# Optimization experiments

Measured on AMD Instinct MI355X. Metric: run time of the kernel, lower is better.

## Reference

```python
import jax, jax.numpy as jnp
import numpy as np

L = 10


def setup_inputs() -> dict:
    key = jax.random.key(0)
    ks = jax.random.split(key, L + 1)
    N = 1_000_000
    inp = {"points": jax.random.normal(ks[0], (N, 3), dtype=jnp.float32)}
    inp["cob_1"] = jax.random.normal(ks[1], (3, 3), dtype=jnp.float32)
    for l in range(2, L + 1):
        # [2l+1, 3*(2l-1)] change-of-basis matrix for angular order l
        inp[f"cob_{l}"] = jax.random.normal(ks[l], (2 * l + 1, 3 * (2 * l - 1)), dtype=jnp.float32)
    return inp


def _harmonic_forward(points, cobs):
    # points: [..., 3]; cobs: list of L matrices (cob_1 .. cob_L)
    shape = points.shape[:-1]
    f0 = jnp.ones(shape + (1,), dtype=points.dtype)
    # order-1 feature: [..., 3]
    f1 = jnp.einsum('...i,ji->...j', points, cobs[0])
    feats = [f0, f1]
    prev = f1
    for l in range(2, L + 1):
        cob = cobs[l - 1]  # [2l+1, 3*(2l-1)]
        # outer product of previous order feature with order-1 feature, flattened
        f = jnp.einsum('...i,...j->...ij', prev, f1).reshape(shape + (-1,))  # [..., 3*(2l-1)]
        f = jnp.einsum('...i,ji->...j', f, cob)  # [..., 2l+1]
        feats.append(f)
        prev = f
    return jnp.concatenate(feats, axis=-1)  # [..., (L+1)^2]


def reference(points, cob_1, cob_2, cob_3, cob_4, cob_5, cob_6, cob_7, cob_8, cob_9, cob_10):
    cobs = [cob_1, cob_2, cob_3, cob_4, cob_5, cob_6, cob_7, cob_8, cob_9, cob_10]
    return _harmonic_forward(points, cobs)
```

## Files before the change

kernel.cpp:

```cpp
#include <hip/hip_runtime.h>

#define BS 64
#define NFEAT 121
#define CHUNK 16
#define NCHUNK 4


__device__ __forceinline__ float dot3(const float* __restrict__ c, float x, float y, float z) {
    return fmaf(c[2], z, fmaf(c[1], y, c[0] * x));
}

template<int LL>
__device__ __forceinline__ void step_l(const float* __restrict__ cob,
                                       float* f, float f1x, float f1y, float f1z) {
    constexpr int IN = 2 * LL - 1;
    constexpr int OUT = 2 * LL + 1;
    constexpr int PB = (LL - 1) * (LL - 1);
    constexpr int OB = LL * LL;
    #pragma unroll
    for (int j = 0; j < OUT; ++j) {
        const float* __restrict__ crow = cob + j * (3 * IN);
        float acc = 0.f;
        #pragma unroll
        for (int a = 0; a < IN; ++a)
            acc = fmaf(f[PB + a], dot3(crow + 3 * a, f1x, f1y, f1z), acc);
        f[OB + j] = acc;
    }
}

__global__ __launch_bounds__(BS) void harmonic_kernel(
    const float* __restrict__ points,
    const float* __restrict__ cob1,  const float* __restrict__ cob2,
    const float* __restrict__ cob3,  const float* __restrict__ cob4,
    const float* __restrict__ cob5,  const float* __restrict__ cob6,
    const float* __restrict__ cob7,  const float* __restrict__ cob8,
    const float* __restrict__ cob9,  const float* __restrict__ cob10,
    float* __restrict__ out, int N) {
    __shared__ float sbuf[CHUNK * NFEAT];

    const int lane = threadIdx.x;
    const long long wbase = (long long)blockIdx.x * BS;
    const long long p = wbase + lane;
    const bool active = p < (long long)N;
    long long nv = (long long)N - wbase;
    const int wrows = nv >= BS ? BS : (nv > 0 ? (int)nv : 0);

    float px = 0.f, py = 0.f, pz = 0.f;
    if (active) {
        px = points[p * 3 + 0];
        py = points[p * 3 + 1];
        pz = points[p * 3 + 2];
    }

    const float f1x = dot3(cob1 + 0, px, py, pz);
    const float f1y = dot3(cob1 + 3, px, py, pz);
    const float f1z = dot3(cob1 + 6, px, py, pz);

    float f[NFEAT];
    f[0] = 1.f; f[1] = f1x; f[2] = f1y; f[3] = f1z;
    step_l<2>(cob2, f, f1x, f1y, f1z);
    step_l<3>(cob3, f, f1x, f1y, f1z);
    step_l<4>(cob4, f, f1x, f1y, f1z);
    step_l<5>(cob5, f, f1x, f1y, f1z);
    step_l<6>(cob6, f, f1x, f1y, f1z);
    step_l<7>(cob7, f, f1x, f1y, f1z);
    step_l<8>(cob8, f, f1x, f1y, f1z);
    step_l<9>(cob9, f, f1x, f1y, f1z);
    step_l<10>(cob10, f, f1x, f1y, f1z);

    float* __restrict__ outw = out + wbase * NFEAT;
    const int myc = lane >> 4;
    const int mr  = lane & 15;

    if (wrows == BS) {
        #pragma unroll 1
        for (int c = 0; c < NCHUNK; ++c) {
            if (myc == c) {
                #pragma unroll
                for (int col = 0; col < NFEAT; ++col)
                    sbuf[mr * NFEAT + col] = f[col];
            }
            const int gbase = c * (CHUNK * NFEAT);
            #pragma unroll
            for (int k = 0; k < 30; ++k)
                outw[gbase + k * 64 + lane] = sbuf[k * 64 + lane];
            if (lane < 16)
                outw[gbase + 1920 + lane] = sbuf[1920 + lane];
        }
    } else if (wrows > 0) {
        #pragma unroll 1
        for (int c = 0; c < NCHUNK; ++c) {
            int vr = wrows - c * CHUNK;
            if (vr <= 0) break;
            if (vr > CHUNK) vr = CHUNK;
            if (myc == c && mr < vr) {
                #pragma unroll
                for (int col = 0; col < NFEAT; ++col)
                    sbuf[mr * NFEAT + col] = f[col];
            }
            const int gbase = c * (CHUNK * NFEAT);
            const int nf = vr * NFEAT;
            #pragma unroll 1
            for (int k = 0; k < 31; ++k) {
                const int idx = k * 64 + lane;
                if (idx < nf) outw[gbase + idx] = sbuf[idx];
            }
        }
    }
}

extern "C" void kernel_launch(void* const* d_in, const int* in_sizes, int n_in,
                              void* d_out, int out_size, void* d_ws, size_t ws_size,
                              hipStream_t stream) {
    const float* points = (const float*)d_in[0];
    const float* cob[10];
    for (int i = 0; i < 10; ++i) cob[i] = (const float*)d_in[1 + i];
    float* out = (float*)d_out;
    const int N = in_sizes[0] / 3;

    const int grid = (N + BS - 1) / BS;
    harmonic_kernel<<<grid, BS, 0, stream>>>(
        points,
        cob[0], cob[1], cob[2], cob[3], cob[4],
        cob[5], cob[6], cob[7], cob[8], cob[9],
        out, N);
}
```

Baseline: 726.1 us.

## Split feature computation into two phases with interleaved shared-memory output staging

```diff
diff --git a/kernel.cpp b/kernel.cpp
--- a/kernel.cpp
+++ b/kernel.cpp
@@ -1,9 +1,12 @@
 #include <hip/hip_runtime.h>
 
-#define BS 64
+#define BS 256
 #define NFEAT 121
 #define CHUNK 16
-#define NCHUNK 4
+#define WA 64
+#define WB 57
+#define SA4 17
+#define SB4 15
 
 
 __device__ __forceinline__ float dot3(const float* __restrict__ c, float x, float y, float z) {
@@ -12,19 +15,18 @@
 
 template<int LL>
 __device__ __forceinline__ void step_l(const float* __restrict__ cob,
-                                       float* f, float f1x, float f1y, float f1z) {
-    constexpr int IN = 2 * LL - 1;
+                                       const float* prevArr, float* outArr,
+                                       float f1x, float f1y, float f1z) {
+    constexpr int IN  = 2 * LL - 1;
     constexpr int OUT = 2 * LL + 1;
-    constexpr int PB = (LL - 1) * (LL - 1);
-    constexpr int OB = LL * LL;
     #pragma unroll
     for (int j = 0; j < OUT; ++j) {
         const float* __restrict__ crow = cob + j * (3 * IN);
         float acc = 0.f;
         #pragma unroll
         for (int a = 0; a < IN; ++a)
-            acc = fmaf(f[PB + a], dot3(crow + 3 * a, f1x, f1y, f1z), acc);
-        f[OB + j] = acc;
+            acc = fmaf(prevArr[a], dot3(crow + 3 * a, f1x, f1y, f1z), acc);
+        outArr[j] = acc;
     }
 }
 
@@ -36,14 +38,16 @@
     const float* __restrict__ cob7,  const float* __restrict__ cob8,
     const float* __restrict__ cob9,  const float* __restrict__ cob10,
     float* __restrict__ out, int N) {
-    __shared__ float sbuf[CHUNK * NFEAT];
+    __shared__ float4 sbuf4[BS / 64][CHUNK * SA4];
 
-    const int lane = threadIdx.x;
-    const long long wbase = (long long)blockIdx.x * BS;
-    const long long p = wbase + lane;
+    const int t    = threadIdx.x;
+    const int lane = t & 63;
+    const int w    = t >> 6;
+    const long long wbase = (long long)blockIdx.x * BS + ((long long)w << 6);
+    const long long p     = wbase + lane;
     const bool active = p < (long long)N;
     long long nv = (long long)N - wbase;
-    const int wrows = nv >= BS ? BS : (nv > 0 ? (int)nv : 0);
+    const int wrows = nv >= 64 ? 64 : (nv > 0 ? (int)nv : 0);
 
     float px = 0.f, py = 0.f, pz = 0.f;
     if (active) {
@@ -56,54 +60,79 @@
     const float f1y = dot3(cob1 + 3, px, py, pz);
     const float f1z = dot3(cob1 + 6, px, py, pz);
 
-    float f[NFEAT];
-    f[0] = 1.f; f[1] = f1x; f[2] = f1y; f[3] = f1z;
-    step_l<2>(cob2, f, f1x, f1y, f1z);
-    step_l<3>(cob3, f, f1x, f1y, f1z);
-    step_l<4>(cob4, f, f1x, f1y, f1z);
-    step_l<5>(cob5, f, f1x, f1y, f1z);
-    step_l<6>(cob6, f, f1x, f1y, f1z);
-    step_l<7>(cob7, f, f1x, f1y, f1z);
-    step_l<8>(cob8, f, f1x, f1y, f1z);
-    step_l<9>(cob9, f, f1x, f1y, f1z);
-    step_l<10>(cob10, f, f1x, f1y, f1z);
+    float4* wb4 = &sbuf4[w][0];
+    float*  wbf = (float*)wb4;
+    float* __restrict__ outw = out + wbase * NFEAT;
 
-    float* __restrict__ outw = out + wbase * NFEAT;
     const int myc = lane >> 4;
     const int mr  = lane & 15;
 
-    if (wrows == BS) {
-        #pragma unroll 1
-        for (int c = 0; c < NCHUNK; ++c) {
+    float fA[WA];
+    fA[0] = 1.f; fA[1] = f1x; fA[2] = f1y; fA[3] = f1z;
+    step_l<2>(cob2, fA + 1,  fA + 4,  f1x, f1y, f1z);
+    step_l<3>(cob3, fA + 4,  fA + 9,  f1x, f1y, f1z);
+    step_l<4>(cob4, fA + 9,  fA + 16, f1x, f1y, f1z);
+    step_l<5>(cob5, fA + 16, fA + 25, f1x, f1y, f1z);
+    step_l<6>(cob6, fA + 25, fA + 36, f1x, f1y, f1z);
+    step_l<7>(cob7, fA + 36, fA + 49, f1x, f1y, f1z);
+
+    if (wrows == 64) {
+        for (int c = 0; c < 4; ++c) {
             if (myc == c) {
                 #pragma unroll
-                for (int col = 0; col < NFEAT; ++col)
-                    sbuf[mr * NFEAT + col] = f[col];
+                for (int k = 0; k < 16; ++k)
+                    wb4[mr * SA4 + k] = make_float4(fA[4*k], fA[4*k+1], fA[4*k+2], fA[4*k+3]);
             }
-            const int gbase = c * (CHUNK * NFEAT);
             #pragma unroll
-            for (int k = 0; k < 30; ++k)
-                outw[gbase + k * 64 + lane] = sbuf[k * 64 + lane];
-            if (lane < 16)
-                outw[gbase + 1920 + lane] = sbuf[1920 + lane];
+            for (int r = 0; r < 16; ++r)
+                outw[(c * 16 + r) * NFEAT + lane] = wbf[r * (4 * SA4) + lane];
         }
     } else if (wrows > 0) {
-        #pragma unroll 1
-        for (int c = 0; c < NCHUNK; ++c) {
-            int vr = wrows - c * CHUNK;
-            if (vr <= 0) break;
-            if (vr > CHUNK) vr = CHUNK;
-            if (myc == c && mr < vr) {
+        for (int c = 0; c < 4 && c * 16 < wrows; ++c) {
+            if (myc == c) {
                 #pragma unroll
-                for (int col = 0; col < NFEAT; ++col)
-                    sbuf[mr * NFEAT + col] = f[col];
+                for (int k = 0; k < 16; ++k)
+                    wb4[mr * SA4 + k] = make_float4(fA[4*k], fA[4*k+1], fA[4*k+2], fA[4*k+3]);
             }
-            const int gbase = c * (CHUNK * NFEAT);
-            const int nf = vr * NFEAT;
-            #pragma unroll 1
-            for (int k = 0; k < 31; ++k) {
-                const int idx = k * 64 + lane;
-                if (idx < nf) outw[gbase + idx] = sbuf[idx];
+            #pragma unroll
+            for (int r = 0; r < 16; ++r)
+                if (c * 16 + r < wrows)
+                    outw[(c * 16 + r) * NFEAT + lane] = wbf[r * (4 * SA4) + lane];
+        }
+    }
+
+    float fB[WB];
+    step_l<8> (cob8,  fA + 49, fB + 0,  f1x, f1y, f1z);
+    step_l<9> (cob9,  fB + 0,  fB + 17, f1x, f1y, f1z);
+    step_l<10>(cob10, fB + 17, fB + 36, f1x, f1y, f1z);
+
+    if (wrows == 64) {
+        for (int c = 0; c < 4; ++c) {
+            if (myc == c) {
+                #pragma unroll
+                for (int k = 0; k < 14; ++k)
+                    wb4[mr * SB4 + k] = make_float4(fB[4*k], fB[4*k+1], fB[4*k+2], fB[4*k+3]);
+                wbf[mr * (4 * SB4) + 56] = fB[56];
+            }
+            if (lane < WB) {
+                #pragma unroll
+                for (int r = 0; r < 16; ++r)
+                    outw[(c * 16 + r) * NFEAT + WA + lane] = wbf[r * (4 * SB4) + lane];
+            }
+        }
+    } else if (wrows > 0) {
+        for (int c = 0; c < 4 && c * 16 < wrows; ++c) {
+            if (myc == c) {
+                #pragma unroll
+                for (int k = 0; k < 14; ++k)
+                    wb4[mr * SB4 + k] = make_float4(fB[4*k], fB[4*k+1], fB[4*k+2], fB[4*k+3]);
+                wbf[mr * (4 * SB4) + 56] = fB[56];
+            }
+            if (lane < WB) {
+                #pragma unroll
+                for (int r = 0; r < 16; ++r)
+                    if (c * 16 + r < wrows)
+                        outw[(c * 16 + r) * NFEAT + WA + lane] = wbf[r * (4 * SB4) + lane];
             }
         }
     }
```

New measurement: 738.4 us. Within noise of the previous version (+1.7%).
